# Optimization experiments

Hardware: AMD Instinct MI355X
Metric: run time of the kernel (lower is better)

Reference implementation:

```python
import jax, jax.numpy as jnp
import numpy as np

ALPHA = 0.1        # ista() default lambda (module-level alpha is unused in this path)
N_ITERS = 50       # fixed iteration count replacing tolerance-based early exit
POWER_ITERS = 20   # power iterations to estimate Lipschitz constant L = ||Wd||_2^2


def _soft_threshold(x, t):
    return jnp.sign(x) * jnp.maximum(jnp.abs(x) - t, 0.0)


def _lipschitz(Wd):
    # largest eigenvalue of Wd^T Wd via power iteration
    v = jnp.ones((Wd.shape[1],), Wd.dtype)
    def body(v, _):
        v = Wd.T @ (Wd @ v)
        v = v / (jnp.linalg.norm(v) + 1e-12)
        return v, None
    v, _ = jax.lax.scan(body, v, None, length=POWER_ITERS)
    return jnp.vdot(v, Wd.T @ (Wd @ v)) / (jnp.vdot(v, v) + 1e-12)


def _ista(X, Wd):
    # X: [B, D], Wd: [D, K] -> sparse codes Z: [B, K]
    L = jax.lax.stop_gradient(_lipschitz(Wd))
    step = 1.0 / L
    Z0 = jnp.zeros((X.shape[0], Wd.shape[1]), X.dtype)
    def body(Z, _):
        grad = (Z @ Wd.T - X) @ Wd          # [B,D] @ [D,K] -> [B,K]
        Z = _soft_threshold(Z - step * grad, step * ALPHA)
        return Z, None
    Z, _ = jax.lax.scan(body, Z0, None, length=N_ITERS)
    return Z


def setup_inputs() -> dict:
    key = jax.random.key(0)
    k1, k2 = jax.random.split(key)
    z_e_x = jax.random.normal(k1, (8192, 16, 8, 8), jnp.float32)   # [B,C,H,W]
    dictionary = jax.random.normal(k2, (1024, 512), jnp.float32)   # [D,K], D=H*W*C
    return {"z_e_x": z_e_x, "dictionary": dictionary}


def reference(z_e_x, dictionary):
    B = z_e_x.shape[0]
    # permute(0,2,3,1).flatten(start_dim=1): [B,C,H,W] -> [B, H*W*C]
    X = jnp.transpose(z_e_x, (0, 2, 3, 1)).reshape(B, -1)
    Z = _ista(X, dictionary)                                  # [B,K]
    sparsity = jnp.sum(jnp.abs(Z) > 1e-6) / B
    outputs = (dictionary @ Z.T).T                            # [B,D]
    # torch code views back to z_e_x.shape WITHOUT inverse permute; replicate exactly
    return outputs.reshape(z_e_x.shape), sparsity
```

## Files before the change

kernel.cpp:

```cpp
#include <hip/hip_runtime.h>
#include <math.h>

#define BATCH 8192
#define DIM 1024
#define KDIM 512
#define ALPHA_C 0.1f
#define N_ITERS 50
#define ROWS 32
#define ZSH 512

typedef short bf16x8 __attribute__((ext_vector_type(8)));
typedef float f32x4 __attribute__((ext_vector_type(4)));

__device__ __forceinline__ short f2bf(float x) {
  union { float f; unsigned u; } v; v.f = x;
  unsigned r = v.u + 0x7fffu + ((v.u >> 16) & 1u);
  return (short)(r >> 16);
}
__device__ __forceinline__ float bf2f(short s) {
  union { float f; unsigned u; } v;
  v.u = ((unsigned)(unsigned short)s) << 16;
  return v.f;
}

__device__ __forceinline__ int zswz(int row, int col) {
  return row * ZSH + ((((col >> 3) ^ (row & 7)) << 3) | (col & 7));
}
__device__ __forceinline__ int zoff8(int row, int colg) {
  return row * ZSH + ((colg ^ (row & 7)) << 3);
}

__global__ __launch_bounds__(256) void k_mmT(const float* __restrict__ A,
                                             const float* __restrict__ B,
                                             float* __restrict__ C, int K,
                                             float scale) {
  int tx = (threadIdx.x & 15) * 2;
  int ty = (threadIdx.x >> 4) * 2;
  int a0 = blockIdx.y * 32 + ty;
  int b0 = blockIdx.x * 32 + tx;
  float a00 = 0.f, a01 = 0.f, a10 = 0.f, a11 = 0.f;
  for (int j = 0; j < K; j += 8) {
#pragma unroll
    for (int u = 0; u < 8; ++u) {
      float2 av = *(const float2*)&A[(size_t)(j + u) * KDIM + a0];
      float2 bv = *(const float2*)&B[(size_t)(j + u) * KDIM + b0];
      a00 += av.x * bv.x;
      a01 += av.x * bv.y;
      a10 += av.y * bv.x;
      a11 += av.y * bv.y;
    }
  }
  *(float2*)&C[(size_t)a0 * KDIM + b0] = make_float2(a00 * scale, a01 * scale);
  *(float2*)&C[(size_t)(a0 + 1) * KDIM + b0] =
      make_float2(a10 * scale, a11 * scale);
}

__global__ __launch_bounds__(1024) void k_power_fast(
    const float* __restrict__ G4, const float* __restrict__ G8,
    const float* __restrict__ G, float* __restrict__ scal) {
  __shared__ float v[KDIM];
  __shared__ float part[1024];
  __shared__ double red[16];
  __shared__ double red2[16];
  __shared__ float stot;
  int tid = threadIdx.x;
  int lane = tid & 63, wid = tid >> 6;
  int col = tid & 511, h = tid >> 9;
  if (h == 0) v[col] = 1.0f;
  __syncthreads();

  const float* mats[3] = {G4, G8, G8};
#pragma unroll
  for (int s = 0; s < 3; ++s) {
    const float* gp = mats[s] + (size_t)(h * 256) * KDIM + col;
    const float* vp = v + h * 256;
    float a0 = 0.f, a1 = 0.f, a2 = 0.f, a3 = 0.f;
#pragma unroll 4
    for (int j = 0; j < 256; j += 4) {
      a0 += gp[(size_t)(j + 0) * KDIM] * vp[j + 0];
      a1 += gp[(size_t)(j + 1) * KDIM] * vp[j + 1];
      a2 += gp[(size_t)(j + 2) * KDIM] * vp[j + 2];
      a3 += gp[(size_t)(j + 3) * KDIM] * vp[j + 3];
    }
    part[tid] = (a0 + a1) + (a2 + a3);
    __syncthreads();
    float u = 0.f;
    double ssq = 0.0;
    if (h == 0) {
      u = part[col] + part[col + 512];
      ssq = (double)u * (double)u;
    }
#pragma unroll
    for (int off = 32; off; off >>= 1) ssq += __shfl_xor(ssq, off);
    if (lane == 0) red[wid] = ssq;
    __syncthreads();
    if (tid == 0) {
      double t = 0.0;
      for (int i = 0; i < 16; ++i) t += red[i];
      stot = (float)(sqrt(t) + 1e-12);
    }
    __syncthreads();
    if (h == 0) v[col] = u / stot;
    __syncthreads();
  }

  {
    const float* gp = G + (size_t)(h * 256) * KDIM + col;
    const float* vp = v + h * 256;
    float a0 = 0.f, a1 = 0.f, a2 = 0.f, a3 = 0.f;
#pragma unroll 4
    for (int j = 0; j < 256; j += 4) {
      a0 += gp[(size_t)(j + 0) * KDIM] * vp[j + 0];
      a1 += gp[(size_t)(j + 1) * KDIM] * vp[j + 1];
      a2 += gp[(size_t)(j + 2) * KDIM] * vp[j + 2];
      a3 += gp[(size_t)(j + 3) * KDIM] * vp[j + 3];
    }
    part[tid] = (a0 + a1) + (a2 + a3);
    __syncthreads();
    double nu = 0.0, de = 0.0;
    if (h == 0) {
      float u = part[col] + part[col + 512];
      nu = (double)v[col] * (double)u;
      de = (double)v[col] * (double)v[col];
    }
#pragma unroll
    for (int off = 32; off; off >>= 1) {
      nu += __shfl_xor(nu, off);
      de += __shfl_xor(de, off);
    }
    if (lane == 0) { red[wid] = nu; red2[wid] = de; }
    __syncthreads();
    if (tid == 0) {
      double n = 0.0, d = 0.0;
      for (int i = 0; i < 16; ++i) { n += red[i]; d += red2[i]; }
      float L = (float)(n / (d + 1e-12));
      float step = 1.0f / L;
      scal[0] = step;
      scal[1] = step * ALPHA_C;
    }
  }
}

__global__ __launch_bounds__(256) void k_pack_h(const float* __restrict__ G,
                                                const float* __restrict__ scal,
                                                short* __restrict__ Hh) {
  int t = blockIdx.x * 256 + threadIdx.x;
  int k = t >> 9, n = t & 511;
  float step = scal[0];
  float h = ((k == n) ? 1.0f : 0.0f) - step * G[k * KDIM + n];
  int kk = k >> 5, q = (k >> 3) & 3, j = k & 7;
  Hh[((size_t)((kk * 4 + q) * 512 + n)) * 8 + j] = f2bf(h);
}

__global__ __launch_bounds__(256) void k_pack_w(const float* __restrict__ Wd,
                                                const float* __restrict__ scal,
                                                short* __restrict__ Wh) {
  int t = blockIdx.x * 256 + threadIdx.x;
  int k = t >> 9, n = t & 511;
  float w = scal[0] * Wd[k * KDIM + n];
  int kk = k >> 5, q = (k >> 3) & 3, j = k & 7;
  Wh[((size_t)((kk * 4 + q) * 512 + n)) * 8 + j] = f2bf(w);
}

__global__ __launch_bounds__(256) void k_pack_wt(const float* __restrict__ Wd,
                                                 short* __restrict__ Wh) {
  int t = blockIdx.x * 256 + threadIdx.x;
  int k = t >> 10, n = t & 1023;
  float w = Wd[n * KDIM + k];
  int kk = k >> 5, q = (k >> 3) & 3, j = k & 7;
  Wh[((size_t)((kk * 4 + q) * 1024 + n)) * 8 + j] = f2bf(w);
}

__global__ __launch_bounds__(1024) void k_ista(
    const float* __restrict__ zex, const short* __restrict__ Hh,
    const short* __restrict__ Wph, const short* __restrict__ Wth,
    const float* __restrict__ scal, float* __restrict__ out,
    int* __restrict__ gcnt) {
  __shared__ short Zb[ROWS * ZSH];
  __shared__ short Zc[ROWS * ZSH];
  int tid = threadIdx.x;
  int lane = tid & 63, wid = tid >> 6;
  int l15 = lane & 15, lq = lane >> 4;
  int rb = blockIdx.x * ROWS;
  float thr = scal[1];

  f32x4 cs[2][2];
#pragma unroll
  for (int rf = 0; rf < 2; ++rf)
#pragma unroll
    for (int cf = 0; cf < 2; ++cf) cs[rf][cf] = (f32x4){0.f, 0.f, 0.f, 0.f};

  int sr = tid >> 5;
  int sc = (tid & 31) >> 1;
  int ph = tid & 1;
  for (int half = 0; half < 2; ++half) {
    __syncthreads();
    {
      const float* src =
          &zex[(size_t)(rb + sr) * DIM + sc * 64 + half * 32 + ph * 16];
#pragma unroll
      for (int m = 0; m < 16; m += 4) {
        float4 xv = *(const float4*)&src[m];
        float xs[4] = {xv.x, xv.y, xv.z, xv.w};
#pragma unroll
        for (int e = 0; e < 4; ++e) {
          int mm = ph * 16 + m + e;
          int dd = ((mm >> 3) << 7) + ((mm & 7) << 4) + sc;
          short hi = f2bf(xs[e]);
          short lo = f2bf(xs[e] - bf2f(hi));
          int zi = zswz(sr, dd);
          Zb[zi] = hi;
          Zc[zi] = lo;
        }
      }
    }
    __syncthreads();
#pragma unroll 2
    for (int kk = 0; kk < 16; ++kk) {
      int kkg = half * 16 + kk;
      bf16x8 ah[2], al[2];
#pragma unroll
      for (int rf = 0; rf < 2; ++rf) {
        int zo = zoff8(rf * 16 + l15, kk * 4 + lq);
        ah[rf] = *(const bf16x8*)&Zb[zo];
        al[rf] = *(const bf16x8*)&Zc[zo];
      }
#pragma unroll
      for (int cf = 0; cf < 2; ++cf) {
        int n = wid * 32 + cf * 16 + l15;
        bf16x8 bh = *(const bf16x8*)&Wph[((size_t)((kkg * 4 + lq) * 512 + n)) * 8];
#pragma unroll
        for (int rf = 0; rf < 2; ++rf) {
          cs[rf][cf] = __builtin_amdgcn_mfma_f32_16x16x32_bf16(ah[rf], bh, cs[rf][cf], 0, 0, 0);
          cs[rf][cf] = __builtin_amdgcn_mfma_f32_16x16x32_bf16(al[rf], bh, cs[rf][cf], 0, 0, 0);
        }
      }
    }
  }
  __syncthreads();

#pragma unroll
  for (int rf = 0; rf < 2; ++rf)
#pragma unroll
    for (int cf = 0; cf < 2; ++cf) {
      int col = wid * 32 + cf * 16 + l15;
#pragma unroll
      for (int e = 0; e < 4; ++e) {
        float pre = cs[rf][cf][e];
        float mag = fmaxf(fabsf(pre) - thr, 0.f);
        float z = (pre >= 0.f) ? mag : -mag;
        int row = rf * 16 + lq * 4 + e;
        Zb[zswz(row, col)] = f2bf(z);
      }
    }
  __syncthreads();

#pragma unroll 1
  for (int it = 1; it < N_ITERS; ++it) {
    int rot = it & 15;
    f32x4 acc[2][2];
#pragma unroll
    for (int rf = 0; rf < 2; ++rf)
#pragma unroll
      for (int cf = 0; cf < 2; ++cf) acc[rf][cf] = cs[rf][cf];

#pragma unroll 2
    for (int kk = 0; kk < 16; ++kk) {
      int kkr = (kk + rot) & 15;
      bf16x8 a[2];
#pragma unroll
      for (int rf = 0; rf < 2; ++rf)
        a[rf] = *(const bf16x8*)&Zb[zoff8(rf * 16 + l15, kkr * 4 + lq)];
#pragma unroll
      for (int cf = 0; cf < 2; ++cf) {
        int n = wid * 32 + cf * 16 + l15;
        bf16x8 bh = *(const bf16x8*)&Hh[((size_t)((kkr * 4 + lq) * 512 + n)) * 8];
#pragma unroll
        for (int rf = 0; rf < 2; ++rf)
          acc[rf][cf] = __builtin_amdgcn_mfma_f32_16x16x32_bf16(a[rf], bh, acc[rf][cf], 0, 0, 0);
      }
    }
    __syncthreads();
#pragma unroll
    for (int rf = 0; rf < 2; ++rf)
#pragma unroll
      for (int cf = 0; cf < 2; ++cf) {
        int col = wid * 32 + cf * 16 + l15;
#pragma unroll
        for (int e = 0; e < 4; ++e) {
          float pre = acc[rf][cf][e];
          float mag = fmaxf(fabsf(pre) - thr, 0.f);
          float z = (pre >= 0.f) ? mag : -mag;
          int row = rf * 16 + lq * 4 + e;
          Zb[zswz(row, col)] = f2bf(z);
        }
      }
    __syncthreads();
  }

  int cnt = 0;
#pragma unroll 4
  for (int i = tid; i < ROWS * ZSH; i += 1024)
    cnt += (fabsf(bf2f(Zb[i])) > 1e-6f) ? 1 : 0;
#pragma unroll
  for (int off = 32; off; off >>= 1) cnt += __shfl_xor(cnt, off);
  if (lane == 0) atomicAdd(gcnt, cnt);

  {
    f32x4 o[2][4];
#pragma unroll
    for (int rf = 0; rf < 2; ++rf)
#pragma unroll
      for (int cf = 0; cf < 4; ++cf) o[rf][cf] = (f32x4){0.f, 0.f, 0.f, 0.f};

#pragma unroll 2
    for (int kk = 0; kk < 16; ++kk) {
      bf16x8 a[2];
#pragma unroll
      for (int rf = 0; rf < 2; ++rf)
        a[rf] = *(const bf16x8*)&Zb[zoff8(rf * 16 + l15, kk * 4 + lq)];
#pragma unroll
      for (int cf = 0; cf < 4; ++cf) {
        int n = wid * 64 + cf * 16 + l15;
        bf16x8 bh = *(const bf16x8*)&Wth[((size_t)((kk * 4 + lq) * 1024 + n)) * 8];
#pragma unroll
        for (int rf = 0; rf < 2; ++rf)
          o[rf][cf] = __builtin_amdgcn_mfma_f32_16x16x32_bf16(a[rf], bh, o[rf][cf], 0, 0, 0);
      }
    }
#pragma unroll
    for (int rf = 0; rf < 2; ++rf)
#pragma unroll
      for (int cf = 0; cf < 4; ++cf) {
        int col = wid * 64 + cf * 16 + l15;
#pragma unroll
        for (int e = 0; e < 4; ++e) {
          int row = rb + rf * 16 + lq * 4 + e;
          out[(size_t)row * DIM + col] = o[rf][cf][e];
        }
      }
  }
}

__global__ void k_final(const int* __restrict__ gcnt, float* __restrict__ out) {
  out[(size_t)BATCH * DIM] = (float)(*gcnt) / (float)BATCH;
}

extern "C" void kernel_launch(void* const* d_in, const int* in_sizes, int n_in,
                              void* d_out, int out_size, void* d_ws,
                              size_t ws_size, hipStream_t stream) {
  (void)in_sizes; (void)n_in; (void)out_size; (void)ws_size;
  const float* zex = (const float*)d_in[0];
  const float* Wd = (const float*)d_in[1];
  float* out = (float*)d_out;
  char* ws = (char*)d_ws;

  float* G = (float*)ws;
  float* G2 = (float*)(ws + (1 << 20));
  float* G4 = (float*)(ws + 2 * (1 << 20));
  float* G8 = (float*)(ws + 3 * (1 << 20));
  short* Hh = (short*)(ws + 4 * (1 << 20));
  short* Wph = (short*)(ws + 4 * (1 << 20) + (512 << 10));
  short* Wth = (short*)(ws + 5 * (1 << 20) + (512 << 10));
  float* scal = (float*)(ws + 6 * (1 << 20) + (512 << 10));
  int* gcnt = (int*)(ws + 6 * (1 << 20) + (512 << 10) + 64);

  hipMemsetAsync(gcnt, 0, sizeof(int), stream);
  dim3 gb(16, 16);
  k_mmT<<<gb, 256, 0, stream>>>(Wd, Wd, G, DIM, 1.0f);
  k_mmT<<<gb, 256, 0, stream>>>(G, G, G2, KDIM, 9.5367431640625e-07f);
  k_mmT<<<gb, 256, 0, stream>>>(G2, G2, G4, KDIM, 1.0f);
  k_mmT<<<gb, 256, 0, stream>>>(G4, G4, G8, KDIM, 1.0f);
  k_power_fast<<<1, 1024, 0, stream>>>(G4, G8, G, scal);
  k_pack_h<<<1024, 256, 0, stream>>>(G, scal, Hh);
  k_pack_w<<<2048, 256, 0, stream>>>(Wd, scal, Wph);
  k_pack_wt<<<2048, 256, 0, stream>>>(Wd, Wth);
  k_ista<<<BATCH / ROWS, 1024, 0, stream>>>(zex, Hh, Wph, Wth, scal, out, gcnt);
  k_final<<<1, 1, 0, stream>>>(gcnt, out);
}
```

Baseline: 543.5 us.

## Double-buffer Z in LDS, cache part of H in LDS, retile Gram matmul

```diff
diff --git a/kernel.cpp b/kernel.cpp
--- a/kernel.cpp
+++ b/kernel.cpp
@@ -8,6 +8,7 @@
 #define N_ITERS 50
 #define ROWS 32
 #define ZSH 512
+#define HC 2
 
 typedef short bf16x8 __attribute__((ext_vector_type(8)));
 typedef float f32x4 __attribute__((ext_vector_type(4)));
@@ -24,35 +25,38 @@
 }
 
 __device__ __forceinline__ int zswz(int row, int col) {
-  return row * ZSH + ((((col >> 3) ^ (row & 7)) << 3) | (col & 7));
+  return row * ZSH + ((((col >> 3) ^ (row & 15)) << 3) | (col & 7));
 }
 __device__ __forceinline__ int zoff8(int row, int colg) {
-  return row * ZSH + ((colg ^ (row & 7)) << 3);
+  return row * ZSH + ((colg ^ (row & 15)) << 3);
 }
 
 __global__ __launch_bounds__(256) void k_mmT(const float* __restrict__ A,
                                              const float* __restrict__ B,
                                              float* __restrict__ C, int K,
                                              float scale) {
-  int tx = (threadIdx.x & 15) * 2;
-  int ty = (threadIdx.x >> 4) * 2;
-  int a0 = blockIdx.y * 32 + ty;
-  int b0 = blockIdx.x * 32 + tx;
-  float a00 = 0.f, a01 = 0.f, a10 = 0.f, a11 = 0.f;
-  for (int j = 0; j < K; j += 8) {
-#pragma unroll
-    for (int u = 0; u < 8; ++u) {
-      float2 av = *(const float2*)&A[(size_t)(j + u) * KDIM + a0];
-      float2 bv = *(const float2*)&B[(size_t)(j + u) * KDIM + b0];
-      a00 += av.x * bv.x;
-      a01 += av.x * bv.y;
-      a10 += av.y * bv.x;
-      a11 += av.y * bv.y;
-    }
-  }
-  *(float2*)&C[(size_t)a0 * KDIM + b0] = make_float2(a00 * scale, a01 * scale);
-  *(float2*)&C[(size_t)(a0 + 1) * KDIM + b0] =
-      make_float2(a10 * scale, a11 * scale);
+  int tx = threadIdx.x & 15;
+  int ty = threadIdx.x >> 4;
+  int a0 = blockIdx.y * 64 + ty * 4;
+  int b0 = blockIdx.x * 64 + tx * 4;
+  float acc[4][4] = {};
+#pragma unroll 4
+  for (int d = 0; d < K; ++d) {
+    float4 av = *(const float4*)&A[(size_t)d * KDIM + a0];
+    float4 bv = *(const float4*)&B[(size_t)d * KDIM + b0];
+    float aa[4] = {av.x, av.y, av.z, av.w};
+    float bb[4] = {bv.x, bv.y, bv.z, bv.w};
+#pragma unroll
+    for (int i = 0; i < 4; ++i)
+#pragma unroll
+      for (int j = 0; j < 4; ++j) acc[i][j] += aa[i] * bb[j];
+  }
+#pragma unroll
+  for (int i = 0; i < 4; ++i) {
+    float4 o = make_float4(acc[i][0] * scale, acc[i][1] * scale,
+                           acc[i][2] * scale, acc[i][3] * scale);
+    *(float4*)&C[(size_t)(a0 + i) * KDIM + b0] = o;
+  }
 }
 
 __global__ __launch_bounds__(1024) void k_power_fast(
@@ -176,8 +180,8 @@
     const short* __restrict__ Wph, const short* __restrict__ Wth,
     const float* __restrict__ scal, float* __restrict__ out,
     int* __restrict__ gcnt) {
-  __shared__ short Zb[ROWS * ZSH];
-  __shared__ short Zc[ROWS * ZSH];
+  __shared__ short Zb[2][ROWS * ZSH];
+  __shared__ short Hl2[HC * 16384];
   int tid = threadIdx.x;
   int lane = tid & 63, wid = tid >> 6;
   int l15 = lane & 15, lq = lane >> 4;
@@ -209,8 +213,8 @@
           short hi = f2bf(xs[e]);
           short lo = f2bf(xs[e] - bf2f(hi));
           int zi = zswz(sr, dd);
-          Zb[zi] = hi;
-          Zc[zi] = lo;
+          Zb[0][zi] = hi;
+          Zb[1][zi] = lo;
         }
       }
     }
@@ -222,8 +226,8 @@
 #pragma unroll
       for (int rf = 0; rf < 2; ++rf) {
         int zo = zoff8(rf * 16 + l15, kk * 4 + lq);
-        ah[rf] = *(const bf16x8*)&Zb[zo];
-        al[rf] = *(const bf16x8*)&Zc[zo];
+        ah[rf] = *(const bf16x8*)&Zb[0][zo];
+        al[rf] = *(const bf16x8*)&Zb[1][zo];
       }
 #pragma unroll
       for (int cf = 0; cf < 2; ++cf) {
@@ -238,6 +242,9 @@
     }
   }
   __syncthreads();
+
+  for (int i = tid * 8; i < HC * 16384; i += 8192)
+    *(bf16x8*)&Hl2[i] = *(const bf16x8*)&Hh[i];
 
 #pragma unroll
   for (int rf = 0; rf < 2; ++rf)
@@ -250,11 +257,12 @@
         float mag = fmaxf(fabsf(pre) - thr, 0.f);
         float z = (pre >= 0.f) ? mag : -mag;
         int row = rf * 16 + lq * 4 + e;
-        Zb[zswz(row, col)] = f2bf(z);
+        Zb[0][zswz(row, col)] = f2bf(z);
       }
     }
   __syncthreads();
 
+  int cur = 0;
 #pragma unroll 1
   for (int it = 1; it < N_ITERS; ++it) {
     int rot = it & 15;
@@ -270,17 +278,19 @@
       bf16x8 a[2];
 #pragma unroll
       for (int rf = 0; rf < 2; ++rf)
-        a[rf] = *(const bf16x8*)&Zb[zoff8(rf * 16 + l15, kkr * 4 + lq)];
+        a[rf] = *(const bf16x8*)&Zb[cur][zoff8(rf * 16 + l15, kkr * 4 + lq)];
 #pragma unroll
       for (int cf = 0; cf < 2; ++cf) {
         int n = wid * 32 + cf * 16 + l15;
-        bf16x8 bh = *(const bf16x8*)&Hh[((size_t)((kkr * 4 + lq) * 512 + n)) * 8];
+        size_t off = ((size_t)((kkr * 4 + lq) * 512 + n)) * 8;
+        bf16x8 bh;
+        if (kkr < HC) bh = *(const bf16x8*)&Hl2[off];
+        else bh = *(const bf16x8*)&Hh[off];
 #pragma unroll
         for (int rf = 0; rf < 2; ++rf)
           acc[rf][cf] = __builtin_amdgcn_mfma_f32_16x16x32_bf16(a[rf], bh, acc[rf][cf], 0, 0, 0);
       }
     }
-    __syncthreads();
 #pragma unroll
     for (int rf = 0; rf < 2; ++rf)
 #pragma unroll
@@ -292,16 +302,17 @@
           float mag = fmaxf(fabsf(pre) - thr, 0.f);
           float z = (pre >= 0.f) ? mag : -mag;
           int row = rf * 16 + lq * 4 + e;
-          Zb[zswz(row, col)] = f2bf(z);
+          Zb[cur ^ 1][zswz(row, col)] = f2bf(z);
         }
       }
+    cur ^= 1;
     __syncthreads();
   }
 
   int cnt = 0;
 #pragma unroll 4
   for (int i = tid; i < ROWS * ZSH; i += 1024)
-    cnt += (fabsf(bf2f(Zb[i])) > 1e-6f) ? 1 : 0;
+    cnt += (fabsf(bf2f(Zb[cur][i])) > 1e-6f) ? 1 : 0;
 #pragma unroll
   for (int off = 32; off; off >>= 1) cnt += __shfl_xor(cnt, off);
   if (lane == 0) atomicAdd(gcnt, cnt);
@@ -318,7 +329,7 @@
       bf16x8 a[2];
 #pragma unroll
       for (int rf = 0; rf < 2; ++rf)
-        a[rf] = *(const bf16x8*)&Zb[zoff8(rf * 16 + l15, kk * 4 + lq)];
+        a[rf] = *(const bf16x8*)&Zb[cur][zoff8(rf * 16 + l15, kk * 4 + lq)];
 #pragma unroll
       for (int cf = 0; cf < 4; ++cf) {
         int n = wid * 64 + cf * 16 + l15;
@@ -366,7 +377,7 @@
   int* gcnt = (int*)(ws + 6 * (1 << 20) + (512 << 10) + 64);
 
   hipMemsetAsync(gcnt, 0, sizeof(int), stream);
-  dim3 gb(16, 16);
+  dim3 gb(8, 8);
   k_mmT<<<gb, 256, 0, stream>>>(Wd, Wd, G, DIM, 1.0f);
   k_mmT<<<gb, 256, 0, stream>>>(G, G, G2, KDIM, 9.5367431640625e-07f);
   k_mmT<<<gb, 256, 0, stream>>>(G2, G2, G4, KDIM, 1.0f);
```

Measured after the change: 610.7 us, median of 4. 1.12x slower.

## Split-K Gram products, double-buffer Z, cache part of H in LDS

Applied to the files above, without the earlier changes.

```diff
diff --git a/kernel.cpp b/kernel.cpp
--- a/kernel.cpp
+++ b/kernel.cpp
@@ -8,6 +8,8 @@
 #define N_ITERS 50
 #define ROWS 32
 #define ZSH 512
+#define HC 3
+#define SEG 256
 
 typedef short bf16x8 __attribute__((ext_vector_type(8)));
 typedef float f32x4 __attribute__((ext_vector_type(4)));
@@ -24,22 +26,22 @@
 }
 
 __device__ __forceinline__ int zswz(int row, int col) {
-  return row * ZSH + ((((col >> 3) ^ (row & 7)) << 3) | (col & 7));
+  return row * ZSH + ((((col >> 3) ^ (row & 15)) << 3) | (col & 7));
 }
 __device__ __forceinline__ int zoff8(int row, int colg) {
-  return row * ZSH + ((colg ^ (row & 7)) << 3);
-}
-
-__global__ __launch_bounds__(256) void k_mmT(const float* __restrict__ A,
-                                             const float* __restrict__ B,
-                                             float* __restrict__ C, int K,
-                                             float scale) {
+  return row * ZSH + ((colg ^ (row & 15)) << 3);
+}
+
+__global__ __launch_bounds__(256) void k_mmT_part(const float* __restrict__ A,
+                                                  const float* __restrict__ B,
+                                                  float* __restrict__ P) {
   int tx = (threadIdx.x & 15) * 2;
   int ty = (threadIdx.x >> 4) * 2;
   int a0 = blockIdx.y * 32 + ty;
   int b0 = blockIdx.x * 32 + tx;
+  int j0 = blockIdx.z * SEG;
   float a00 = 0.f, a01 = 0.f, a10 = 0.f, a11 = 0.f;
-  for (int j = 0; j < K; j += 8) {
+  for (int j = j0; j < j0 + SEG; j += 8) {
 #pragma unroll
     for (int u = 0; u < 8; ++u) {
       float2 av = *(const float2*)&A[(size_t)(j + u) * KDIM + a0];
@@ -50,9 +52,22 @@
       a11 += av.y * bv.y;
     }
   }
-  *(float2*)&C[(size_t)a0 * KDIM + b0] = make_float2(a00 * scale, a01 * scale);
-  *(float2*)&C[(size_t)(a0 + 1) * KDIM + b0] =
-      make_float2(a10 * scale, a11 * scale);
+  float* P0 = P + (size_t)blockIdx.z * KDIM * KDIM;
+  *(float2*)&P0[(size_t)a0 * KDIM + b0] = make_float2(a00, a01);
+  *(float2*)&P0[(size_t)(a0 + 1) * KDIM + b0] = make_float2(a10, a11);
+}
+
+__global__ __launch_bounds__(256) void k_red(const float* __restrict__ P,
+                                             float* __restrict__ C, int S,
+                                             float scale) {
+  int t = blockIdx.x * 256 + threadIdx.x;
+  f32x4 s = (f32x4){0.f, 0.f, 0.f, 0.f};
+  for (int z = 0; z < S; ++z) {
+    f32x4 p = *(const f32x4*)&P[(size_t)z * KDIM * KDIM + t * 4];
+    s.x += p.x; s.y += p.y; s.z += p.z; s.w += p.w;
+  }
+  s.x *= scale; s.y *= scale; s.z *= scale; s.w *= scale;
+  *(f32x4*)&C[t * 4] = s;
 }
 
 __global__ __launch_bounds__(1024) void k_power_fast(
@@ -176,8 +191,8 @@
     const short* __restrict__ Wph, const short* __restrict__ Wth,
     const float* __restrict__ scal, float* __restrict__ out,
     int* __restrict__ gcnt) {
-  __shared__ short Zb[ROWS * ZSH];
-  __shared__ short Zc[ROWS * ZSH];
+  __shared__ short Zb[2][ROWS * ZSH];
+  __shared__ short Hl2[HC * 16384];
   int tid = threadIdx.x;
   int lane = tid & 63, wid = tid >> 6;
   int l15 = lane & 15, lq = lane >> 4;
@@ -206,11 +221,7 @@
         for (int e = 0; e < 4; ++e) {
           int mm = ph * 16 + m + e;
           int dd = ((mm >> 3) << 7) + ((mm & 7) << 4) + sc;
-          short hi = f2bf(xs[e]);
-          short lo = f2bf(xs[e] - bf2f(hi));
-          int zi = zswz(sr, dd);
-          Zb[zi] = hi;
-          Zc[zi] = lo;
+          Zb[0][zswz(sr, dd)] = f2bf(xs[e]);
         }
       }
     }
@@ -218,26 +229,24 @@
 #pragma unroll 2
     for (int kk = 0; kk < 16; ++kk) {
       int kkg = half * 16 + kk;
-      bf16x8 ah[2], al[2];
-#pragma unroll
-      for (int rf = 0; rf < 2; ++rf) {
-        int zo = zoff8(rf * 16 + l15, kk * 4 + lq);
-        ah[rf] = *(const bf16x8*)&Zb[zo];
-        al[rf] = *(const bf16x8*)&Zc[zo];
-      }
+      bf16x8 a[2];
+#pragma unroll
+      for (int rf = 0; rf < 2; ++rf)
+        a[rf] = *(const bf16x8*)&Zb[0][zoff8(rf * 16 + l15, kk * 4 + lq)];
 #pragma unroll
       for (int cf = 0; cf < 2; ++cf) {
         int n = wid * 32 + cf * 16 + l15;
         bf16x8 bh = *(const bf16x8*)&Wph[((size_t)((kkg * 4 + lq) * 512 + n)) * 8];
 #pragma unroll
-        for (int rf = 0; rf < 2; ++rf) {
-          cs[rf][cf] = __builtin_amdgcn_mfma_f32_16x16x32_bf16(ah[rf], bh, cs[rf][cf], 0, 0, 0);
-          cs[rf][cf] = __builtin_amdgcn_mfma_f32_16x16x32_bf16(al[rf], bh, cs[rf][cf], 0, 0, 0);
-        }
+        for (int rf = 0; rf < 2; ++rf)
+          cs[rf][cf] = __builtin_amdgcn_mfma_f32_16x16x32_bf16(a[rf], bh, cs[rf][cf], 0, 0, 0);
       }
     }
   }
   __syncthreads();
+
+  for (int i = tid * 8; i < HC * 16384; i += 8192)
+    *(bf16x8*)&Hl2[i] = *(const bf16x8*)&Hh[i];
 
 #pragma unroll
   for (int rf = 0; rf < 2; ++rf)
@@ -250,37 +259,52 @@
         float mag = fmaxf(fabsf(pre) - thr, 0.f);
         float z = (pre >= 0.f) ? mag : -mag;
         int row = rf * 16 + lq * 4 + e;
-        Zb[zswz(row, col)] = f2bf(z);
+        Zb[0][zswz(row, col)] = f2bf(z);
       }
     }
   __syncthreads();
 
+  int cur = 0;
 #pragma unroll 1
   for (int it = 1; it < N_ITERS; ++it) {
     int rot = it & 15;
     f32x4 acc[2][2];
-#pragma unroll
-    for (int rf = 0; rf < 2; ++rf)
-#pragma unroll
-      for (int cf = 0; cf < 2; ++cf) acc[rf][cf] = cs[rf][cf];
-
+
+    {
+      int kkr = rot;
+      bf16x8 a[2];
+#pragma unroll
+      for (int rf = 0; rf < 2; ++rf)
+        a[rf] = *(const bf16x8*)&Zb[cur][zoff8(rf * 16 + l15, kkr * 4 + lq)];
+#pragma unroll
+      for (int cf = 0; cf < 2; ++cf) {
+        int n = wid * 32 + cf * 16 + l15;
+        size_t off = ((size_t)((kkr * 4 + lq) * 512 + n)) * 8;
+        bf16x8 bh = (kkr < HC) ? *(const bf16x8*)&Hl2[off]
+                               : *(const bf16x8*)&Hh[off];
+#pragma unroll
+        for (int rf = 0; rf < 2; ++rf)
+          acc[rf][cf] = __builtin_amdgcn_mfma_f32_16x16x32_bf16(a[rf], bh, cs[rf][cf], 0, 0, 0);
+      }
+    }
 #pragma unroll 2
-    for (int kk = 0; kk < 16; ++kk) {
+    for (int kk = 1; kk < 16; ++kk) {
       int kkr = (kk + rot) & 15;
       bf16x8 a[2];
 #pragma unroll
       for (int rf = 0; rf < 2; ++rf)
-        a[rf] = *(const bf16x8*)&Zb[zoff8(rf * 16 + l15, kkr * 4 + lq)];
+        a[rf] = *(const bf16x8*)&Zb[cur][zoff8(rf * 16 + l15, kkr * 4 + lq)];
 #pragma unroll
       for (int cf = 0; cf < 2; ++cf) {
         int n = wid * 32 + cf * 16 + l15;
-        bf16x8 bh = *(const bf16x8*)&Hh[((size_t)((kkr * 4 + lq) * 512 + n)) * 8];
+        size_t off = ((size_t)((kkr * 4 + lq) * 512 + n)) * 8;
+        bf16x8 bh = (kkr < HC) ? *(const bf16x8*)&Hl2[off]
+                               : *(const bf16x8*)&Hh[off];
 #pragma unroll
         for (int rf = 0; rf < 2; ++rf)
           acc[rf][cf] = __builtin_amdgcn_mfma_f32_16x16x32_bf16(a[rf], bh, acc[rf][cf], 0, 0, 0);
       }
     }
-    __syncthreads();
 #pragma unroll
     for (int rf = 0; rf < 2; ++rf)
 #pragma unroll
@@ -292,16 +316,17 @@
           float mag = fmaxf(fabsf(pre) - thr, 0.f);
           float z = (pre >= 0.f) ? mag : -mag;
           int row = rf * 16 + lq * 4 + e;
-          Zb[zswz(row, col)] = f2bf(z);
+          Zb[cur ^ 1][zswz(row, col)] = f2bf(z);
         }
       }
+    cur ^= 1;
     __syncthreads();
   }
 
   int cnt = 0;
 #pragma unroll 4
   for (int i = tid; i < ROWS * ZSH; i += 1024)
-    cnt += (fabsf(bf2f(Zb[i])) > 1e-6f) ? 1 : 0;
+    cnt += (fabsf(bf2f(Zb[cur][i])) > 1e-6f) ? 1 : 0;
 #pragma unroll
   for (int off = 32; off; off >>= 1) cnt += __shfl_xor(cnt, off);
   if (lane == 0) atomicAdd(gcnt, cnt);
@@ -318,7 +343,7 @@
       bf16x8 a[2];
 #pragma unroll
       for (int rf = 0; rf < 2; ++rf)
-        a[rf] = *(const bf16x8*)&Zb[zoff8(rf * 16 + l15, kk * 4 + lq)];
+        a[rf] = *(const bf16x8*)&Zb[cur][zoff8(rf * 16 + l15, kk * 4 + lq)];
 #pragma unroll
       for (int cf = 0; cf < 4; ++cf) {
         int n = wid * 64 + cf * 16 + l15;
@@ -364,13 +389,20 @@
   short* Wth = (short*)(ws + 5 * (1 << 20) + (512 << 10));
   float* scal = (float*)(ws + 6 * (1 << 20) + (512 << 10));
   int* gcnt = (int*)(ws + 6 * (1 << 20) + (512 << 10) + 64);
+  float* PG = (float*)(ws + 1 * (1 << 20));
+  float* PG2 = (float*)(ws + 2 * (1 << 20));
+  float* PG4 = (float*)(ws + 3 * (1 << 20));
+  float* PG8 = (float*)(ws + 4 * (1 << 20));
 
   hipMemsetAsync(gcnt, 0, sizeof(int), stream);
-  dim3 gb(16, 16);
-  k_mmT<<<gb, 256, 0, stream>>>(Wd, Wd, G, DIM, 1.0f);
-  k_mmT<<<gb, 256, 0, stream>>>(G, G, G2, KDIM, 9.5367431640625e-07f);
-  k_mmT<<<gb, 256, 0, stream>>>(G2, G2, G4, KDIM, 1.0f);
-  k_mmT<<<gb, 256, 0, stream>>>(G4, G4, G8, KDIM, 1.0f);
+  k_mmT_part<<<dim3(16, 16, 4), 256, 0, stream>>>(Wd, Wd, PG);
+  k_red<<<256, 256, 0, stream>>>(PG, G, 4, 1.0f);
+  k_mmT_part<<<dim3(16, 16, 2), 256, 0, stream>>>(G, G, PG2);
+  k_red<<<256, 256, 0, stream>>>(PG2, G2, 2, 9.5367431640625e-07f);
+  k_mmT_part<<<dim3(16, 16, 2), 256, 0, stream>>>(G2, G2, PG4);
+  k_red<<<256, 256, 0, stream>>>(PG4, G4, 2, 1.0f);
+  k_mmT_part<<<dim3(16, 16, 2), 256, 0, stream>>>(G4, G4, PG8);
+  k_red<<<256, 256, 0, stream>>>(PG8, G8, 2, 1.0f);
   k_power_fast<<<1, 1024, 0, stream>>>(G4, G8, G, scal);
   k_pack_h<<<1024, 256, 0, stream>>>(G, scal, Hh);
   k_pack_w<<<2048, 256, 0, stream>>>(Wd, scal, Wph);
```

Result: no change. 545.6 us (+0.4%).
